# Optimization experiments

Measured on AMD Instinct MI355X. Metric: run time of the kernel, lower is better.

The kernel has to match this reference:

```python
import math
import jax, jax.numpy as jnp
import numpy as np

NUM_HEADS = 8

def setup_inputs() -> dict:
    key = jax.random.key(0)
    ks = jax.random.split(key, 4)
    b, c, T, H, W = 8, 512, 8, 16, 16
    data_dim = T * H * W  # 2048
    x = jax.random.normal(ks[0], (b, c, T, H, W), dtype=jnp.float32)
    pos_emb = jax.random.normal(ks[1], (c, data_dim + 1), dtype=jnp.float32) / math.sqrt(c)
    w_qkv = jax.random.normal(ks[2], (3 * c, c), dtype=jnp.float32) * (1.0 / math.sqrt(c))
    b_qkv = jnp.zeros((3 * c,), dtype=jnp.float32)
    w_c = jax.random.normal(ks[3], (c, c), dtype=jnp.float32) * (1.0 / math.sqrt(c))
    b_c = jnp.zeros((c,), dtype=jnp.float32)
    return {"x": x, "pos_emb": pos_emb, "w_qkv": w_qkv, "b_qkv": b_qkv, "w_c": w_c, "b_c": b_c}

def reference(x, pos_emb, w_qkv, b_qkv, w_c, b_c):
    b, c = x.shape[0], x.shape[1]
    xf = x.reshape(b, c, -1)                                   # [b, c, THW]
    xf = jnp.concatenate([xf.mean(axis=-1, keepdims=True), xf], axis=-1)  # [b, c, T+1]
    xf = xf + pos_emb[None].astype(xf.dtype)
    qkv = jnp.einsum('oc,bct->bot', w_qkv, xf) + b_qkv[None, :, None]      # [b, 3c, L]
    L = qkv.shape[-1]
    ch = c // NUM_HEADS
    q, k, v = jnp.split(qkv, 3, axis=1)
    q = q.reshape(b * NUM_HEADS, ch, L)
    k = k.reshape(b * NUM_HEADS, ch, L)
    v = v.reshape(b * NUM_HEADS, ch, L)
    scale = 1.0 / math.sqrt(math.sqrt(ch))
    w = jnp.einsum('bct,bcs->bts', q * scale, k * scale)        # [bH, L, L]
    w = jax.nn.softmax(w.astype(jnp.float32), axis=-1).astype(qkv.dtype)
    a = jnp.einsum('bts,bcs->bct', w, v).reshape(b, c, L)       # [b, c, L]
    out = jnp.einsum('oc,bct->bot', w_c, a) + b_c[None, :, None]
    return out[:, :, 0]                                         # [b, out_dim]
```

## Files before the change

kernel.cpp:

```cpp
#include <hip/hip_runtime.h>

#define B 8
#define C 512
#define D 2048
#define L 2049
#define NH 8
#define CH 64

__device__ __forceinline__ float wave_reduce_sum(float v) {
  #pragma unroll
  for (int off = 32; off; off >>= 1) v += __shfl_down(v, off);
  return v;
}

__global__ void __launch_bounds__(256) k_mean(const float* __restrict__ x, float* __restrict__ mean) {
  int row = blockIdx.x;
  const float4* xr = reinterpret_cast<const float4*>(x + (size_t)row * D);
  float s = 0.f;
  #pragma unroll
  for (int i = 0; i < 2; ++i) {
    float4 v = xr[threadIdx.x + i * 256];
    s += (v.x + v.y) + (v.z + v.w);
  }
  __shared__ float red[4];
  s = wave_reduce_sum(s);
  if ((threadIdx.x & 63) == 0) red[threadIdx.x >> 6] = s;
  __syncthreads();
  if (threadIdx.x == 0) mean[row] = (red[0] + red[1] + red[2] + red[3]) * (1.0f / D);
}

__global__ void __launch_bounds__(256) k_qu(const float* __restrict__ wqkv,
                                            const float* __restrict__ pos,
                                            const float* __restrict__ mean,
                                            float* __restrict__ u,
                                            float* __restrict__ logit0) {
  int bh = blockIdx.x, b = bh >> 3, h = bh & 7;
  int tid = threadIdx.x, wid = tid >> 6, lane = tid & 63;
  __shared__ float mps[C];
  __shared__ float q0s[CH];
  __shared__ float us[C];
  __shared__ float red[4];
  for (int c = tid; c < C; c += 256) mps[c] = mean[b * C + c] + pos[(size_t)c * L];
  __syncthreads();
  for (int j = wid; j < CH; j += 4) {
    const float* wr = wqkv + (size_t)(h * CH + j) * C;
    float acc = 0.f;
    for (int c = lane; c < C; c += 64) acc += wr[c] * mps[c];
    acc = wave_reduce_sum(acc);
    if (lane == 0) q0s[j] = acc;
  }
  __syncthreads();
  __syncthreads();
  float a0 = 0.f, a1 = 0.f;
  for (int j = 0; j < CH; ++j) {
    float qv = q0s[j];
    const float* wkr = wqkv + (size_t)(C + h * CH + j) * C;
    a0 += qv * wkr[tid];
    a1 += qv * wkr[tid + 256];
  }
  a0 *= 0.125f; a1 *= 0.125f;
  us[tid] = a0; us[tid + 256] = a1;
  u[(size_t)bh * C + tid] = a0;
  u[(size_t)bh * C + tid + 256] = a1;
  __syncthreads();
  float p = us[tid] * mps[tid] + us[tid + 256] * mps[tid + 256];
  p = wave_reduce_sum(p);
  if (lane == 0) red[wid] = p;
  __syncthreads();
  if (tid == 0) logit0[bh] = red[0] + red[1] + red[2] + red[3];
}

__global__ void __launch_bounds__(256) k_qu2(const float* __restrict__ wqkv,
                                             const float* __restrict__ bqkv,
                                             const float* __restrict__ pos,
                                             const float* __restrict__ mean,
                                             float* __restrict__ u,
                                             float* __restrict__ logit0) {
  int bh = blockIdx.x, b = bh >> 3, h = bh & 7;
  int tid = threadIdx.x, wid = tid >> 6, lane = tid & 63;
  __shared__ float mps[C];
  __shared__ float q0s[CH];
  __shared__ float us[C];
  __shared__ float red[4];
  for (int c = tid; c < C; c += 256) mps[c] = mean[b * C + c] + pos[(size_t)c * L];
  __syncthreads();
  for (int j = wid; j < CH; j += 4) {
    const float* wr = wqkv + (size_t)(h * CH + j) * C;
    float acc = 0.f;
    for (int c = lane; c < C; c += 64) acc += wr[c] * mps[c];
    acc = wave_reduce_sum(acc);
    if (lane == 0) q0s[j] = acc + bqkv[h * CH + j];
  }
  __syncthreads();
  float a0 = 0.f, a1 = 0.f;
  for (int j = 0; j < CH; ++j) {
    float qv = q0s[j];
    const float* wkr = wqkv + (size_t)(C + h * CH + j) * C;
    a0 += qv * wkr[tid];
    a1 += qv * wkr[tid + 256];
  }
  a0 *= 0.125f; a1 *= 0.125f;
  us[tid] = a0; us[tid + 256] = a1;
  u[(size_t)bh * C + tid] = a0;
  u[(size_t)bh * C + tid + 256] = a1;
  __syncthreads();
  float p = us[tid] * mps[tid] + us[tid + 256] * mps[tid + 256];
  p = wave_reduce_sum(p);
  if (lane == 0) red[wid] = p;
  __syncthreads();
  if (tid == 0) logit0[bh] = red[0] + red[1] + red[2] + red[3];
}

__global__ void __launch_bounds__(256) k_logits(const float* __restrict__ x,
                                                const float* __restrict__ pos,
                                                const float* __restrict__ u,
                                                float* __restrict__ wpart) {
  __shared__ float ulds[NH][256];
  __shared__ float rlds[4][NH][128];
  int b = blockIdx.y, bz = blockIdx.z;
  int tid = threadIdx.x, wid = tid >> 6, lane = tid & 63;
  for (int idx = tid; idx < NH * 256; idx += 256) {
    int h = idx >> 8, cc = idx & 255;
    ulds[h][cc] = u[(size_t)(b * NH + h) * C + bz * 256 + cc];
  }
  __syncthreads();
  int l0 = blockIdx.x * 128 + lane * 2;
  int cg = bz * 256 + wid * 64;
  const float* xp = x + ((size_t)(b * C + cg)) * D + l0;
  const float* pp = pos + (size_t)cg * L + l0 + 1;
  float2 acc[NH];
  #pragma unroll
  for (int h = 0; h < NH; ++h) acc[h] = make_float2(0.f, 0.f);
  #pragma unroll 4
  for (int cc = 0; cc < 64; ++cc) {
    float2 xv = *reinterpret_cast<const float2*>(xp);
    float v0 = xv.x + pp[0];
    float v1 = xv.y + pp[1];
    #pragma unroll
    for (int h = 0; h < NH; ++h) {
      float uu = ulds[h][wid * 64 + cc];
      acc[h].x += uu * v0;
      acc[h].y += uu * v1;
    }
    xp += D; pp += L;
  }
  #pragma unroll
  for (int h = 0; h < NH; ++h) {
    rlds[wid][h][lane * 2]     = acc[h].x;
    rlds[wid][h][lane * 2 + 1] = acc[h].y;
  }
  __syncthreads();
  for (int idx = tid; idx < NH * 128; idx += 256) {
    int h = idx >> 7, ll = idx & 127;
    float s = rlds[0][h][ll] + rlds[1][h][ll] + rlds[2][h][ll] + rlds[3][h][ll];
    wpart[((size_t)(bz * B * NH) + b * NH + h) * (size_t)D + blockIdx.x * 128 + ll] = s;
  }
}

__global__ void __launch_bounds__(256) k_softmax(const float* __restrict__ wpart,
                                                 const float* __restrict__ logit0,
                                                 float* __restrict__ wrow,
                                                 float* __restrict__ w0) {
  int bh = blockIdx.x, tid = threadIdx.x, wid = tid >> 6, lane = tid & 63;
  __shared__ float vv[D];
  __shared__ float red[4];
  __shared__ float bc;
  const float* r0 = wpart + (size_t)bh * D;
  const float* r1 = wpart + (size_t)(B * NH + bh) * D;
  float lg0 = logit0[bh];
  float m = lg0;
  for (int i = tid; i < D; i += 256) {
    float v = r0[i] + r1[i];
    vv[i] = v;
    m = fmaxf(m, v);
  }
  #pragma unroll
  for (int off = 32; off; off >>= 1) m = fmaxf(m, __shfl_down(m, off));
  if (lane == 0) red[wid] = m;
  __syncthreads();
  if (tid == 0) bc = fmaxf(fmaxf(red[0], red[1]), fmaxf(red[2], red[3]));
  __syncthreads();
  float M = bc;
  float s = 0.f;
  for (int i = tid; i < D; i += 256) { float e = __expf(vv[i] - M); vv[i] = e; s += e; }
  float e0 = __expf(lg0 - M);
  s = wave_reduce_sum(s);
  __syncthreads();
  if (lane == 0) red[wid] = s;
  __syncthreads();
  if (tid == 0) bc = red[0] + red[1] + red[2] + red[3] + e0;
  __syncthreads();
  float inv = 1.0f / bc;
  for (int i = tid; i < D; i += 256) wrow[(size_t)bh * D + i] = vv[i] * inv;
  if (tid == 0) w0[bh] = e0 * inv;
}

__global__ void __launch_bounds__(256) k_xbar(const float* __restrict__ x,
                                              const float* __restrict__ pos,
                                              const float* __restrict__ mean,
                                              const float* __restrict__ wrow,
                                              const float* __restrict__ w0,
                                              float* __restrict__ xbar) {
  int tid = threadIdx.x, wid = tid >> 6, lane = tid & 63;
  int gw = blockIdx.x * 4 + wid;
  int b = gw >> 7;
  int c0 = (gw & 127) * 4;
  float acc[4][NH];
  #pragma unroll
  for (int cl = 0; cl < 4; ++cl)
    #pragma unroll
    for (int h = 0; h < NH; ++h) acc[cl][h] = 0.f;
  for (int it = 0; it < 8; ++it) {
    int i4 = it * 64 + lane;
    float4 wv[NH];
    #pragma unroll
    for (int h = 0; h < NH; ++h)
      wv[h] = reinterpret_cast<const float4*>(wrow + (size_t)(b * NH + h) * D)[i4];
    #pragma unroll
    for (int cl = 0; cl < 4; ++cl) {
      int c = c0 + cl;
      float4 xv = reinterpret_cast<const float4*>(x + (size_t)(b * C + c) * D)[i4];
      const float* pp = pos + (size_t)c * L + 1 + i4 * 4;
      float v0 = xv.x + pp[0], v1 = xv.y + pp[1], v2 = xv.z + pp[2], v3 = xv.w + pp[3];
      #pragma unroll
      for (int h = 0; h < NH; ++h)
        acc[cl][h] += wv[h].x * v0 + wv[h].y * v1 + wv[h].z * v2 + wv[h].w * v3;
    }
  }
  #pragma unroll
  for (int cl = 0; cl < 4; ++cl) {
    int c = c0 + cl;
    float m0 = (lane == 0) ? (mean[b * C + c] + pos[(size_t)c * L]) : 0.f;
    #pragma unroll
    for (int h = 0; h < NH; ++h) {
      float a = acc[cl][h] + m0 * w0[b * NH + h];
      a = wave_reduce_sum(a);
      if (lane == 0) xbar[(size_t)(b * NH + h) * C + c] = a;
    }
  }
}

__global__ void __launch_bounds__(256) k_a0(const float* __restrict__ wqkv, const float* __restrict__ bqkv,
                                            const float* __restrict__ xbar, float* __restrict__ a0) {
  int gw = blockIdx.x * 4 + (threadIdx.x >> 6);
  int lane = threadIdx.x & 63;
  int b = gw >> 9;
  int cv = gw & 511;
  int h = cv >> 6;
  float acc = 0.f;
  const float* wr = wqkv + (size_t)(2 * C + cv) * C;
  const float* xb = xbar + (size_t)(b * NH + h) * C;
  for (int c = lane; c < C; c += 64) acc += wr[c] * xb[c];
  acc = wave_reduce_sum(acc);
  if (lane == 0) a0[b * C + cv] = acc + bqkv[2 * C + cv];
}

__global__ void __launch_bounds__(256) k_out(const float* __restrict__ wc, const float* __restrict__ bc,
                                             const float* __restrict__ a0, float* __restrict__ out) {
  int gw = blockIdx.x * 4 + (threadIdx.x >> 6);
  int lane = threadIdx.x & 63;
  int b = gw >> 9;
  int o = gw & 511;
  float acc = 0.f;
  const float* wr = wc + (size_t)o * C;
  const float* ar = a0 + b * C;
  for (int c = lane; c < C; c += 64) acc += wr[c] * ar[c];
  acc = wave_reduce_sum(acc);
  if (lane == 0) out[b * C + o] = acc + bc[o];
}

extern "C" void kernel_launch(void* const* d_in, const int* in_sizes, int n_in,
                              void* d_out, int out_size, void* d_ws, size_t ws_size,
                              hipStream_t stream) {
  const float* x    = (const float*)d_in[0];
  const float* pos  = (const float*)d_in[1];
  const float* wqkv = (const float*)d_in[2];
  const float* bqkv = (const float*)d_in[3];
  const float* wc   = (const float*)d_in[4];
  const float* bc   = (const float*)d_in[5];
  float* out = (float*)d_out;
  float* ws  = (float*)d_ws;

  float* mean   = ws;
  float* u      = ws + 4096;
  float* logit0 = ws + 36864;
  float* wpart  = ws + 36928;
  float* wrow   = ws + 299072;
  float* w0     = ws + 430144;
  float* xbar   = ws + 430208;
  float* a0     = ws + 462976;

  hipLaunchKernelGGL(k_mean,    dim3(B * C),       dim3(256), 0, stream, x, mean);
  hipLaunchKernelGGL(k_qu2,     dim3(B * NH),      dim3(256), 0, stream, wqkv, bqkv, pos, mean, u, logit0);
  hipLaunchKernelGGL(k_logits,  dim3(16, B, 2),    dim3(256), 0, stream, x, pos, u, wpart);
  hipLaunchKernelGGL(k_softmax, dim3(B * NH),      dim3(256), 0, stream, wpart, logit0, wrow, w0);
  hipLaunchKernelGGL(k_xbar,    dim3(256),         dim3(256), 0, stream, x, pos, mean, wrow, w0, xbar);
  hipLaunchKernelGGL(k_a0,      dim3(B * C / 4),   dim3(256), 0, stream, wqkv, bqkv, xbar, a0);
  hipLaunchKernelGGL(k_out,     dim3(B * C / 4),   dim3(256), 0, stream, wc, bc, a0, out);
}
```

Measured before the change: 69.99 us.

## Fuse logits, softmax and value reduction into a flash-style split-softmax kernel

Result: faster. 62.82 us (-10.2%).

```diff
diff --git a/kernel.cpp b/kernel.cpp
--- a/kernel.cpp
+++ b/kernel.cpp
@@ -6,10 +6,17 @@
 #define L 2049
 #define NH 8
 #define CH 64
-
-__device__ __forceinline__ float wave_reduce_sum(float v) {
+#define NLT 32
+#define TLD 513
+
+__device__ __forceinline__ float wave_sum(float v) {
   #pragma unroll
   for (int off = 32; off; off >>= 1) v += __shfl_down(v, off);
+  return v;
+}
+__device__ __forceinline__ float wave_max(float v) {
+  #pragma unroll
+  for (int off = 32; off; off >>= 1) v = fmaxf(v, __shfl_down(v, off));
   return v;
 }
 
@@ -23,13 +30,14 @@
     s += (v.x + v.y) + (v.z + v.w);
   }
   __shared__ float red[4];
-  s = wave_reduce_sum(s);
+  s = wave_sum(s);
   if ((threadIdx.x & 63) == 0) red[threadIdx.x >> 6] = s;
   __syncthreads();
   if (threadIdx.x == 0) mean[row] = (red[0] + red[1] + red[2] + red[3]) * (1.0f / D);
 }
 
 __global__ void __launch_bounds__(256) k_qu(const float* __restrict__ wqkv,
+                                            const float* __restrict__ bqkv,
                                             const float* __restrict__ pos,
                                             const float* __restrict__ mean,
                                             float* __restrict__ u,
@@ -45,13 +53,14 @@
   for (int j = wid; j < CH; j += 4) {
     const float* wr = wqkv + (size_t)(h * CH + j) * C;
     float acc = 0.f;
-    for (int c = lane; c < C; c += 64) acc += wr[c] * mps[c];
-    acc = wave_reduce_sum(acc);
-    if (lane == 0) q0s[j] = acc;
-  }
-  __syncthreads();
+    #pragma unroll
+    for (int k = 0; k < 8; ++k) acc += wr[lane + k * 64] * mps[lane + k * 64];
+    acc = wave_sum(acc);
+    if (lane == 0) q0s[j] = acc + bqkv[h * CH + j];
+  }
   __syncthreads();
   float a0 = 0.f, a1 = 0.f;
+  #pragma unroll 4
   for (int j = 0; j < CH; ++j) {
     float qv = q0s[j];
     const float* wkr = wqkv + (size_t)(C + h * CH + j) * C;
@@ -64,209 +73,147 @@
   u[(size_t)bh * C + tid + 256] = a1;
   __syncthreads();
   float p = us[tid] * mps[tid] + us[tid + 256] * mps[tid + 256];
-  p = wave_reduce_sum(p);
+  p = wave_sum(p);
   if (lane == 0) red[wid] = p;
   __syncthreads();
   if (tid == 0) logit0[bh] = red[0] + red[1] + red[2] + red[3];
 }
 
-__global__ void __launch_bounds__(256) k_qu2(const float* __restrict__ wqkv,
-                                             const float* __restrict__ bqkv,
-                                             const float* __restrict__ pos,
-                                             const float* __restrict__ mean,
-                                             float* __restrict__ u,
-                                             float* __restrict__ logit0) {
+__global__ void __launch_bounds__(512, 1) k_fused_lx(
+    const float* __restrict__ x, const float* __restrict__ pos,
+    const float* __restrict__ u_g,
+    float* __restrict__ xpart, float* __restrict__ mpart, float* __restrict__ spart) {
+  __shared__ float tile[64][TLD];
+  __shared__ float rlds[8][NH][64];
+  __shared__ float e_lds[NH][64];
+  int lt = blockIdx.x, b = blockIdx.y;
+  int tid = threadIdx.x, wid = tid >> 6, lane = tid & 63;
+  int cg = wid * 64;
+  int col = lt * 64 + lane;
+
+  float ureg[NH];
+  #pragma unroll
+  for (int h = 0; h < NH; ++h) ureg[h] = u_g[(size_t)(b * NH + h) * C + cg + lane];
+
+  float acc[NH];
+  #pragma unroll
+  for (int h = 0; h < NH; ++h) acc[h] = 0.f;
+
+  const float* xp = x + ((size_t)(b * C + cg)) * D + col;
+  const float* pp = pos + (size_t)cg * L + col + 1;
+  #pragma unroll 4
+  for (int cc = 0; cc < 64; ++cc) {
+    float v = *xp + *pp;
+    tile[lane][cg + cc] = v;
+    xp += D; pp += L;
+    #pragma unroll
+    for (int h = 0; h < NH; ++h) acc[h] += __shfl(ureg[h], cc) * v;
+  }
+  #pragma unroll
+  for (int h = 0; h < NH; ++h) rlds[wid][h][lane] = acc[h];
+  __syncthreads();
+
+  {
+    int h = wid;
+    float lg = 0.f;
+    #pragma unroll
+    for (int w = 0; w < 8; ++w) lg += rlds[w][h][lane];
+    float m = wave_max(lg);
+    m = __shfl(m, 0);
+    float e = __expf(lg - m);
+    float s = wave_sum(e);
+    e_lds[h][lane] = e;
+    if (lane == 0) {
+      mpart[(b * NH + h) * NLT + lt] = m;
+      spart[(b * NH + h) * NLT + lt] = s;
+    }
+  }
+  __syncthreads();
+
+  float a2[NH];
+  #pragma unroll
+  for (int h = 0; h < NH; ++h) a2[h] = 0.f;
+  #pragma unroll 4
+  for (int l = 0; l < 64; ++l) {
+    float xv = tile[l][tid];
+    #pragma unroll
+    for (int h = 0; h < NH; ++h) a2[h] += e_lds[h][l] * xv;
+  }
+  #pragma unroll
+  for (int h = 0; h < NH; ++h)
+    xpart[(((size_t)b * NLT + lt) * NH + h) * C + tid] = a2[h];
+}
+
+__global__ void __launch_bounds__(512) k_comb_a0(
+    const float* __restrict__ xpart, const float* __restrict__ mpart,
+    const float* __restrict__ spart, const float* __restrict__ logit0,
+    const float* __restrict__ mean, const float* __restrict__ pos,
+    const float* __restrict__ wqkv, const float* __restrict__ bqkv,
+    float* __restrict__ a0v) {
   int bh = blockIdx.x, b = bh >> 3, h = bh & 7;
   int tid = threadIdx.x, wid = tid >> 6, lane = tid & 63;
-  __shared__ float mps[C];
-  __shared__ float q0s[CH];
-  __shared__ float us[C];
-  __shared__ float red[4];
-  for (int c = tid; c < C; c += 256) mps[c] = mean[b * C + c] + pos[(size_t)c * L];
-  __syncthreads();
-  for (int j = wid; j < CH; j += 4) {
-    const float* wr = wqkv + (size_t)(h * CH + j) * C;
-    float acc = 0.f;
-    for (int c = lane; c < C; c += 64) acc += wr[c] * mps[c];
-    acc = wave_reduce_sum(acc);
-    if (lane == 0) q0s[j] = acc + bqkv[h * CH + j];
-  }
-  __syncthreads();
-  float a0 = 0.f, a1 = 0.f;
-  for (int j = 0; j < CH; ++j) {
-    float qv = q0s[j];
-    const float* wkr = wqkv + (size_t)(C + h * CH + j) * C;
-    a0 += qv * wkr[tid];
-    a1 += qv * wkr[tid + 256];
-  }
-  a0 *= 0.125f; a1 *= 0.125f;
-  us[tid] = a0; us[tid + 256] = a1;
-  u[(size_t)bh * C + tid] = a0;
-  u[(size_t)bh * C + tid + 256] = a1;
-  __syncthreads();
-  float p = us[tid] * mps[tid] + us[tid + 256] * mps[tid + 256];
-  p = wave_reduce_sum(p);
-  if (lane == 0) red[wid] = p;
-  __syncthreads();
-  if (tid == 0) logit0[bh] = red[0] + red[1] + red[2] + red[3];
-}
-
-__global__ void __launch_bounds__(256) k_logits(const float* __restrict__ x,
-                                                const float* __restrict__ pos,
-                                                const float* __restrict__ u,
-                                                float* __restrict__ wpart) {
-  __shared__ float ulds[NH][256];
-  __shared__ float rlds[4][NH][128];
-  int b = blockIdx.y, bz = blockIdx.z;
-  int tid = threadIdx.x, wid = tid >> 6, lane = tid & 63;
-  for (int idx = tid; idx < NH * 256; idx += 256) {
-    int h = idx >> 8, cc = idx & 255;
-    ulds[h][cc] = u[(size_t)(b * NH + h) * C + bz * 256 + cc];
-  }
-  __syncthreads();
-  int l0 = blockIdx.x * 128 + lane * 2;
-  int cg = bz * 256 + wid * 64;
-  const float* xp = x + ((size_t)(b * C + cg)) * D + l0;
-  const float* pp = pos + (size_t)cg * L + l0 + 1;
-  float2 acc[NH];
-  #pragma unroll
-  for (int h = 0; h < NH; ++h) acc[h] = make_float2(0.f, 0.f);
-  #pragma unroll 4
-  for (int cc = 0; cc < 64; ++cc) {
-    float2 xv = *reinterpret_cast<const float2*>(xp);
-    float v0 = xv.x + pp[0];
-    float v1 = xv.y + pp[1];
-    #pragma unroll
-    for (int h = 0; h < NH; ++h) {
-      float uu = ulds[h][wid * 64 + cc];
-      acc[h].x += uu * v0;
-      acc[h].y += uu * v1;
-    }
-    xp += D; pp += L;
-  }
-  #pragma unroll
-  for (int h = 0; h < NH; ++h) {
-    rlds[wid][h][lane * 2]     = acc[h].x;
-    rlds[wid][h][lane * 2 + 1] = acc[h].y;
-  }
-  __syncthreads();
-  for (int idx = tid; idx < NH * 128; idx += 256) {
-    int h = idx >> 7, ll = idx & 127;
-    float s = rlds[0][h][ll] + rlds[1][h][ll] + rlds[2][h][ll] + rlds[3][h][ll];
-    wpart[((size_t)(bz * B * NH) + b * NH + h) * (size_t)D + blockIdx.x * 128 + ll] = s;
-  }
-}
-
-__global__ void __launch_bounds__(256) k_softmax(const float* __restrict__ wpart,
-                                                 const float* __restrict__ logit0,
-                                                 float* __restrict__ wrow,
-                                                 float* __restrict__ w0) {
-  int bh = blockIdx.x, tid = threadIdx.x, wid = tid >> 6, lane = tid & 63;
-  __shared__ float vv[D];
-  __shared__ float red[4];
-  __shared__ float bc;
-  const float* r0 = wpart + (size_t)bh * D;
-  const float* r1 = wpart + (size_t)(B * NH + bh) * D;
+  __shared__ float row[C];
+  __shared__ float rr[NLT];
+  __shared__ float Msh, Sinv;
   float lg0 = logit0[bh];
-  float m = lg0;
-  for (int i = tid; i < D; i += 256) {
-    float v = r0[i] + r1[i];
-    vv[i] = v;
-    m = fmaxf(m, v);
-  }
-  #pragma unroll
-  for (int off = 32; off; off >>= 1) m = fmaxf(m, __shfl_down(m, off));
-  if (lane == 0) red[wid] = m;
-  __syncthreads();
-  if (tid == 0) bc = fmaxf(fmaxf(red[0], red[1]), fmaxf(red[2], red[3]));
-  __syncthreads();
-  float M = bc;
-  float s = 0.f;
-  for (int i = tid; i < D; i += 256) { float e = __expf(vv[i] - M); vv[i] = e; s += e; }
-  float e0 = __expf(lg0 - M);
-  s = wave_reduce_sum(s);
-  __syncthreads();
-  if (lane == 0) red[wid] = s;
-  __syncthreads();
-  if (tid == 0) bc = red[0] + red[1] + red[2] + red[3] + e0;
-  __syncthreads();
-  float inv = 1.0f / bc;
-  for (int i = tid; i < D; i += 256) wrow[(size_t)bh * D + i] = vv[i] * inv;
-  if (tid == 0) w0[bh] = e0 * inv;
-}
-
-__global__ void __launch_bounds__(256) k_xbar(const float* __restrict__ x,
-                                              const float* __restrict__ pos,
-                                              const float* __restrict__ mean,
-                                              const float* __restrict__ wrow,
-                                              const float* __restrict__ w0,
-                                              float* __restrict__ xbar) {
-  int tid = threadIdx.x, wid = tid >> 6, lane = tid & 63;
-  int gw = blockIdx.x * 4 + wid;
-  int b = gw >> 7;
-  int c0 = (gw & 127) * 4;
-  float acc[4][NH];
-  #pragma unroll
-  for (int cl = 0; cl < 4; ++cl)
-    #pragma unroll
-    for (int h = 0; h < NH; ++h) acc[cl][h] = 0.f;
-  for (int it = 0; it < 8; ++it) {
-    int i4 = it * 64 + lane;
-    float4 wv[NH];
-    #pragma unroll
-    for (int h = 0; h < NH; ++h)
-      wv[h] = reinterpret_cast<const float4*>(wrow + (size_t)(b * NH + h) * D)[i4];
-    #pragma unroll
-    for (int cl = 0; cl < 4; ++cl) {
-      int c = c0 + cl;
-      float4 xv = reinterpret_cast<const float4*>(x + (size_t)(b * C + c) * D)[i4];
-      const float* pp = pos + (size_t)c * L + 1 + i4 * 4;
-      float v0 = xv.x + pp[0], v1 = xv.y + pp[1], v2 = xv.z + pp[2], v3 = xv.w + pp[3];
-      #pragma unroll
-      for (int h = 0; h < NH; ++h)
-        acc[cl][h] += wv[h].x * v0 + wv[h].y * v1 + wv[h].z * v2 + wv[h].w * v3;
-    }
-  }
-  #pragma unroll
-  for (int cl = 0; cl < 4; ++cl) {
-    int c = c0 + cl;
-    float m0 = (lane == 0) ? (mean[b * C + c] + pos[(size_t)c * L]) : 0.f;
-    #pragma unroll
-    for (int h = 0; h < NH; ++h) {
-      float a = acc[cl][h] + m0 * w0[b * NH + h];
-      a = wave_reduce_sum(a);
-      if (lane == 0) xbar[(size_t)(b * NH + h) * C + c] = a;
-    }
-  }
-}
-
-__global__ void __launch_bounds__(256) k_a0(const float* __restrict__ wqkv, const float* __restrict__ bqkv,
-                                            const float* __restrict__ xbar, float* __restrict__ a0) {
-  int gw = blockIdx.x * 4 + (threadIdx.x >> 6);
-  int lane = threadIdx.x & 63;
-  int b = gw >> 9;
-  int cv = gw & 511;
-  int h = cv >> 6;
+  if (tid < NLT) rr[tid] = mpart[bh * NLT + tid];
+  __syncthreads();
+  if (tid == 0) {
+    float M = lg0;
+    #pragma unroll
+    for (int t = 0; t < NLT; ++t) M = fmaxf(M, rr[t]);
+    Msh = M;
+  }
+  __syncthreads();
+  float M = Msh;
+  if (tid < NLT) rr[tid] = __expf(rr[tid] - M);
+  __syncthreads();
+  if (tid == 0) {
+    float S = __expf(lg0 - M);
+    #pragma unroll
+    for (int t = 0; t < NLT; ++t) S += spart[bh * NLT + t] * rr[t];
+    Sinv = 1.0f / S;
+  }
   float acc = 0.f;
-  const float* wr = wqkv + (size_t)(2 * C + cv) * C;
-  const float* xb = xbar + (size_t)(b * NH + h) * C;
-  for (int c = lane; c < C; c += 64) acc += wr[c] * xb[c];
-  acc = wave_reduce_sum(acc);
-  if (lane == 0) a0[b * C + cv] = acc + bqkv[2 * C + cv];
-}
-
-__global__ void __launch_bounds__(256) k_out(const float* __restrict__ wc, const float* __restrict__ bc,
-                                             const float* __restrict__ a0, float* __restrict__ out) {
-  int gw = blockIdx.x * 4 + (threadIdx.x >> 6);
-  int lane = threadIdx.x & 63;
-  int b = gw >> 9;
-  int o = gw & 511;
-  float acc = 0.f;
-  const float* wr = wc + (size_t)o * C;
-  const float* ar = a0 + b * C;
-  for (int c = lane; c < C; c += 64) acc += wr[c] * ar[c];
-  acc = wave_reduce_sum(acc);
-  if (lane == 0) out[b * C + o] = acc + bc[o];
+  #pragma unroll 4
+  for (int t = 0; t < NLT; ++t)
+    acc += xpart[(((size_t)b * NLT + t) * NH + h) * C + tid] * rr[t];
+  float xf0 = mean[b * C + tid] + pos[(size_t)tid * L];
+  acc += __expf(lg0 - M) * xf0;
+  __syncthreads();
+  row[tid] = acc * Sinv;
+  __syncthreads();
+  #pragma unroll 2
+  for (int j = 0; j < 8; ++j) {
+    int o = h * CH + wid * 8 + j;
+    const float* wr = wqkv + (size_t)(2 * C + o) * C;
+    float d = 0.f;
+    #pragma unroll
+    for (int k = 0; k < 8; ++k) d += wr[lane + k * 64] * row[lane + k * 64];
+    d = wave_sum(d);
+    if (lane == 0) a0v[b * C + o] = d + bqkv[2 * C + o];
+  }
+}
+
+__global__ void __launch_bounds__(512) k_out(const float* __restrict__ wc,
+                                             const float* __restrict__ bc,
+                                             const float* __restrict__ a0v,
+                                             float* __restrict__ out) {
+  int bid = blockIdx.x, b = bid >> 3, og = (bid & 7) * 64;
+  int tid = threadIdx.x, wid = tid >> 6, lane = tid & 63;
+  __shared__ float row[C];
+  row[tid] = a0v[b * C + tid];
+  __syncthreads();
+  #pragma unroll 2
+  for (int j = 0; j < 8; ++j) {
+    int o = og + wid * 8 + j;
+    const float* wr = wc + (size_t)o * C;
+    float d = 0.f;
+    #pragma unroll
+    for (int k = 0; k < 8; ++k) d += wr[lane + k * 64] * row[lane + k * 64];
+    d = wave_sum(d);
+    if (lane == 0) out[b * C + o] = d + bc[o];
+  }
 }
 
 extern "C" void kernel_launch(void* const* d_in, const int* in_sizes, int n_in,
@@ -284,17 +231,15 @@
   float* mean   = ws;
   float* u      = ws + 4096;
   float* logit0 = ws + 36864;
-  float* wpart  = ws + 36928;
-  float* wrow   = ws + 299072;
-  float* w0     = ws + 430144;
-  float* xbar   = ws + 430208;
-  float* a0     = ws + 462976;
-
-  hipLaunchKernelGGL(k_mean,    dim3(B * C),       dim3(256), 0, stream, x, mean);
-  hipLaunchKernelGGL(k_qu2,     dim3(B * NH),      dim3(256), 0, stream, wqkv, bqkv, pos, mean, u, logit0);
-  hipLaunchKernelGGL(k_logits,  dim3(16, B, 2),    dim3(256), 0, stream, x, pos, u, wpart);
-  hipLaunchKernelGGL(k_softmax, dim3(B * NH),      dim3(256), 0, stream, wpart, logit0, wrow, w0);
-  hipLaunchKernelGGL(k_xbar,    dim3(256),         dim3(256), 0, stream, x, pos, mean, wrow, w0, xbar);
-  hipLaunchKernelGGL(k_a0,      dim3(B * C / 4),   dim3(256), 0, stream, wqkv, bqkv, xbar, a0);
-  hipLaunchKernelGGL(k_out,     dim3(B * C / 4),   dim3(256), 0, stream, wc, bc, a0, out);
-}
+  float* mpart  = ws + 36928;
+  float* spart  = ws + 38976;
+  float* a0v    = ws + 41024;
+  float* xpart  = ws + 45120;
+
+  hipLaunchKernelGGL(k_mean,     dim3(B * C),    dim3(256), 0, stream, x, mean);
+  hipLaunchKernelGGL(k_qu,       dim3(B * NH),   dim3(256), 0, stream, wqkv, bqkv, pos, mean, u, logit0);
+  hipLaunchKernelGGL(k_fused_lx, dim3(NLT, B),   dim3(512), 0, stream, x, pos, u, xpart, mpart, spart);
+  hipLaunchKernelGGL(k_comb_a0,  dim3(B * NH),   dim3(512), 0, stream, xpart, mpart, spart, logit0,
+                     mean, pos, wqkv, bqkv, a0v);
+  hipLaunchKernelGGL(k_out,      dim3(B * NH),   dim3(512), 0, stream, wc, bc, a0v, out);
+}
```
